# Optimization experiments

Hardware: AMD Instinct MI355X
Metric: run time of the kernel (lower is better)

The kernel has to match this reference:

```python
import jax, jax.numpy as jnp
import numpy as np

S, B, D, H = 1024, 16, 512, 8
DH = D // H  # 64


def setup_inputs() -> dict:
    key = jax.random.key(0)
    k1, k2, k3, k4, k5 = jax.random.split(key, 5)
    x = jax.random.normal(k1, (S, B, D), dtype=jnp.float32)
    # binary validity mask [B, S]: 1 = keep, 0 = masked out (matches torch usage)
    mask = (jax.random.uniform(k2, (B, S)) > 0.2).astype(jnp.float32)
    scale = 1.0 / np.sqrt(D)
    wq = jax.random.normal(k3, (H, DH, D), dtype=jnp.float32) * scale
    wk = jax.random.normal(k4, (H, DH, D), dtype=jnp.float32) * scale
    wv = jax.random.normal(k5, (H, DH, D), dtype=jnp.float32) * scale
    return {"x": x, "mask": mask, "wq": wq, "wk": wk, "wv": wv}


def reference(x, mask, wq, wk, wv):
    # x: [S, B, D]; mask: [B, S]; w*: [H, DH, D] (stacked bias-free Linear weights)
    dh = wq.shape[1]
    # per-hop projections for all hops at once (Linear: y = x @ W.T)
    q = jnp.einsum('sbd,hed->bhse', x, wq)  # [B,H,S,DH]
    k = jnp.einsum('sbd,hed->bhse', x, wk)
    v = jnp.einsum('sbd,hed->bhse', x, wv)
    scores = jnp.einsum('bhse,bhte->bhst', q, k)  # [B,H,S,S]
    inv_mask = (1.0 - mask)[:, None, None, :]      # broadcast over heads, query pos
    align = jnp.tanh(scores / jnp.sqrt(jnp.asarray(dh, x.dtype))) - 10000.0 * inv_mask
    align = jax.nn.softmax(align, axis=-1)
    out = jnp.einsum('bhst,bhte->bhse', align, v)  # [B,H,S,DH]
    s, b = x.shape[0], x.shape[1]
    # concat hops along feature dim, back to seq-first: [S, B, H*DH]
    return jnp.transpose(out, (2, 0, 1, 3)).reshape(s, b, -1)
```

## Files before the change

### kernel.cpp

```cpp
#include <hip/hip_runtime.h>
#include <stdint.h>
#include <stddef.h>

#define SS 1024
#define BB 16
#define DD 512
#define HH 8
#define DHH 64

typedef __attribute__((ext_vector_type(8))) short bf16x8;
typedef __attribute__((ext_vector_type(4))) float f32x4;
typedef __attribute__((ext_vector_type(16))) float f32x16;
typedef __attribute__((ext_vector_type(4))) float float4v;
typedef __attribute__((ext_vector_type(4))) unsigned short us4;

__device__ __forceinline__ unsigned short f2bf(float f) {
  union { float f; unsigned int u; } v; v.f = f;
  unsigned int x = v.u;
  return (unsigned short)((x + 0x7FFFu + ((x >> 16) & 1u)) >> 16);
}

#define GLDS16(dst, src)                                                                  \
  __builtin_amdgcn_global_load_lds(                                                      \
      (const __attribute__((address_space(1))) unsigned int*)(const void*)(src),         \
      (__attribute__((address_space(3))) unsigned int*)(void*)(dst), 16, 0, 0)

__global__ void cvt_kernel(const float* __restrict__ x,
                           const float* __restrict__ wq,
                           const float* __restrict__ wk,
                           const float* __restrict__ wv,
                           const float* __restrict__ mask,
                           unsigned short* __restrict__ xb,
                           unsigned short* __restrict__ wb,
                           float* __restrict__ maskq) {
  const int i = blockIdx.x * 256 + threadIdx.x;
  const int n_x4 = (SS * BB * DD) / 4;
  const int n_w4 = 3 * 65536;
  if (i < n_x4) {
    float4v v = ((const float4v*)x)[i];
    us4 o;
    o[0] = f2bf(v[0]); o[1] = f2bf(v[1]); o[2] = f2bf(v[2]); o[3] = f2bf(v[3]);
    ((us4*)xb)[i] = o;
  } else if (i < n_x4 + n_w4) {
    const int j = i - n_x4;
    const int sel = j >> 16;
    const int off4 = j & 65535;
    const float* wsrc = (sel == 0) ? wq : ((sel == 1) ? wk : wv);
    const float scale = (sel == 0) ? 0.36067376022224085f : 1.0f;
    float4v v = ((const float4v*)wsrc)[off4];
    us4 o;
    o[0] = f2bf(v[0] * scale); o[1] = f2bf(v[1] * scale);
    o[2] = f2bf(v[2] * scale); o[3] = f2bf(v[3] * scale);
    ((us4*)wb)[(sel << 16) + off4] = o;
  } else {
    const int j = i - n_x4 - n_w4;
    float4v mv = ((const float4v*)mask)[j];
    float4v o;
#pragma unroll
    for (int c = 0; c < 4; ++c) o[c] = (mv[c] > 0.5f) ? 0.f : -16384.f;
    ((float4v*)maskq)[j] = o;
  }
}

__global__ __launch_bounds__(256) void proj_kernel(
    const unsigned short* __restrict__ xb,
    const unsigned short* __restrict__ wb,
    unsigned short* __restrict__ qb,
    unsigned short* __restrict__ kb,
    unsigned short* __restrict__ vt) {
  const int bm = blockIdx.x * 128;
  const int bn = blockIdx.y * 128;
  const int b = blockIdx.z / 3;
  const int wsel = blockIdx.z % 3;

  __shared__ unsigned short At[128 * 32];
  __shared__ unsigned short Bt[128 * 32];
  __shared__ unsigned short OT[4][64 * 72];

  const int tid = threadIdx.x;
  const int w = tid >> 6;
  const int lane = tid & 63;

  const unsigned short* wptr = wb + wsel * (512 * DD);

  f32x4 acc[4][4];
#pragma unroll
  for (int mi = 0; mi < 4; ++mi)
#pragma unroll
    for (int ni = 0; ni < 4; ++ni) acc[mi][ni] = (f32x4){0.f, 0.f, 0.f, 0.f};

  const int m0 = (w & 1) * 64;
  const int n0 = (w >> 1) * 64;

  for (int kt = 0; kt < 16; ++kt) {
#pragma unroll
    for (int i = 0; i < 2; ++i) {
      const int idx8 = i * 256 + tid;
      const int r = idx8 >> 2;
      const int c8 = idx8 & 3;
      GLDS16(&At[(i * 256 + w * 64) * 8],
             xb + (size_t)(bm + r) * (BB * DD) + b * DD + kt * 32 + c8 * 8);
      GLDS16(&Bt[(i * 256 + w * 64) * 8],
             wptr + (size_t)(bn + r) * DD + kt * 32 + c8 * 8);
    }
    __syncthreads();
    bf16x8 af[4], bfr[4];
#pragma unroll
    for (int mi = 0; mi < 4; ++mi)
      af[mi] = *(const bf16x8*)&At[(m0 + mi * 16 + (lane & 15)) * 32 + (lane >> 4) * 8];
#pragma unroll
    for (int ni = 0; ni < 4; ++ni)
      bfr[ni] = *(const bf16x8*)&Bt[(n0 + ni * 16 + (lane & 15)) * 32 + (lane >> 4) * 8];
#pragma unroll
    for (int mi = 0; mi < 4; ++mi)
#pragma unroll
      for (int ni = 0; ni < 4; ++ni)
        acc[mi][ni] =
            __builtin_amdgcn_mfma_f32_16x16x32_bf16(af[mi], bfr[ni], acc[mi][ni], 0, 0, 0);
    __syncthreads();
  }

  const int h = (bn + n0) >> 6;
  unsigned short* OTw = &OT[w][0];
  if (wsel != 2) {
#pragma unroll
    for (int mi = 0; mi < 4; ++mi)
#pragma unroll
      for (int ni = 0; ni < 4; ++ni)
#pragma unroll
        for (int j = 0; j < 4; ++j)
          OTw[(mi * 16 + (lane >> 4) * 4 + j) * 72 + ni * 16 + (lane & 15)] =
              f2bf(acc[mi][ni][j]);
  } else {
#pragma unroll
    for (int mi = 0; mi < 4; ++mi)
#pragma unroll
      for (int ni = 0; ni < 4; ++ni) {
        us4 pk;
#pragma unroll
        for (int j = 0; j < 4; ++j) pk[j] = f2bf(acc[mi][ni][j]);
        *(us4*)&OTw[(ni * 16 + (lane & 15)) * 72 + mi * 16 + (lane >> 4) * 4] = pk;
      }
  }
  unsigned short* gout = (wsel == 0) ? qb : ((wsel == 1) ? kb : vt);
#pragma unroll
  for (int pass = 0; pass < 8; ++pass) {
    const int row = pass * 8 + (lane >> 3);
    bf16x8 vrow = *(const bf16x8*)&OTw[row * 72 + (lane & 7) * 8];
    size_t dst;
    if (wsel != 2)
      dst = ((size_t)(b * HH + h) * SS + (size_t)(bm + m0 + row)) * DHH + (lane & 7) * 8;
    else
      dst = ((size_t)(b * HH + h) * DHH + (size_t)row) * SS + (bm + m0) + (lane & 7) * 8;
    *(bf16x8*)&gout[dst] = vrow;
  }
}

__global__ __launch_bounds__(256, 4) void attn_kernel(
    const unsigned short* __restrict__ qb,
    const unsigned short* __restrict__ kb,
    const unsigned short* __restrict__ vt,
    const float* __restrict__ maskq,
    float* __restrict__ out) {
  const int id = blockIdx.x;
  const int xcd = id & 7;
  const int slot = id >> 3;
  const int bh = xcd * 16 + (slot >> 3);
  const int qt = slot & 7;
  const int b = bh >> 3;
  const int h = bh & 7;
  const int tid = threadIdx.x;
  const int w = tid >> 6;
  const int lane = tid & 63;
  const int l31 = lane & 31;
  const int hi32 = lane >> 5;

  __shared__ unsigned short Ks[2][64 * 64];
  __shared__ unsigned short Vs[2][64 * 64];
  __shared__ float rs_s[4][32];

  const size_t base_qk = (size_t)bh * SS * DHH;
  const int q0 = qt * 128 + w * 32;

  bf16x8 aq[4];
  {
    const unsigned short* qp = qb + base_qk + (size_t)(q0 + l31) * DHH + hi32 * 8;
    aq[0] = *(const bf16x8*)(qp);
    aq[1] = *(const bf16x8*)(qp + 16);
    aq[2] = *(const bf16x8*)(qp + 32);
    aq[3] = *(const bf16x8*)(qp + 48);
  }

  const int sr0 = w * 16 + (lane >> 3);
  const int sxb = (((lane & 7) ^ (lane >> 3)) << 4);
  const unsigned short* ksrc0 = kb + base_qk + (size_t)sr0 * DHH + (sxb >> 1);
  const unsigned short* ksrc1 = ksrc0 + 8 * DHH;
  const unsigned short* vsrc0 =
      vt + (size_t)bh * DHH * SS + (size_t)sr0 * SS + (sxb >> 1);
  const unsigned short* vsrc1 = vsrc0 + 8 * SS;

#define STAGE(bb, kt2)                                                       \
  do {                                                                       \
    GLDS16(&Ks[bb][(w * 16) * 64], ksrc0 + (size_t)(kt2) * (64 * DHH));      \
    GLDS16(&Ks[bb][(w * 16 + 8) * 64], ksrc1 + (size_t)(kt2) * (64 * DHH));  \
    GLDS16(&Vs[bb][(w * 16) * 64], vsrc0 + (size_t)(kt2) * 64);              \
    GLDS16(&Vs[bb][(w * 16 + 8) * 64], vsrc1 + (size_t)(kt2) * 64);          \
  } while (0)

  STAGE(0, 0);

  f32x16 accO[2];
#pragma unroll
  for (int n = 0; n < 2; ++n)
#pragma unroll
    for (int i = 0; i < 16; ++i) accO[n][i] = 0.f;
  float rs = 0.f;
  const float* mrow = maskq + b * SS;

  __syncthreads();

  int buf = 0;
  for (int kt = 0; kt < 16; ++kt) {
    if (kt < 15) STAGE(buf ^ 1, kt + 1);
    const char* Kb = (const char*)&Ks[buf][0];
    const char* Vb = (const char*)&Vs[buf][0];

#pragma unroll
    for (int T = 0; T < 2; ++T) {
      const int krow = T * 32 + l31;
      const int ksw = (krow & 7) << 4;
      f32x16 sc = {};
#pragma unroll
      for (int ks = 0; ks < 4; ++ks) {
        bf16x8 kf = *(const bf16x8*)(Kb + krow * 128 + ((ks * 32 + hi32 * 16) ^ ksw));
        sc = __builtin_amdgcn_mfma_f32_32x32x16_bf16(kf, aq[ks], sc, 0, 0, 0);
      }
      unsigned int pu[16];
#pragma unroll
      for (int g = 0; g < 4; ++g) {
        float4v mv = *(const float4v*)&mrow[kt * 64 + T * 32 + g * 8 + hi32 * 4];
#pragma unroll
        for (int i = 0; i < 4; ++i) {
          float u = __builtin_amdgcn_exp2f(sc[g * 4 + i]);
          float r = __builtin_amdgcn_rcpf(1.f + u);
          float p = __builtin_amdgcn_exp2f(__builtin_fmaf(r, -2.88539008178f, mv[i]));
          rs += p;
          union { float f; unsigned int u; } cv;
          cv.f = p;
          pu[g * 4 + i] = cv.u;
        }
      }
      unsigned int wv[8];
#pragma unroll
      for (int m = 0; m < 8; ++m)
        wv[m] = __builtin_amdgcn_perm(pu[2 * m + 1], pu[2 * m], 0x07060302u);
      unsigned int t0 = hi32 ? wv[0] : wv[2];
      unsigned int t1 = hi32 ? wv[1] : wv[3];
      unsigned int t2 = hi32 ? wv[4] : wv[6];
      unsigned int t3 = hi32 ? wv[5] : wv[7];
      unsigned int s0 = (unsigned int)__shfl_xor((int)t0, 32, 64);
      unsigned int s1 = (unsigned int)__shfl_xor((int)t1, 32, 64);
      unsigned int s2 = (unsigned int)__shfl_xor((int)t2, 32, 64);
      unsigned int s3 = (unsigned int)__shfl_xor((int)t3, 32, 64);
      union { unsigned int u[4]; bf16x8 v; } f0, f1;
      f0.u[0] = hi32 ? s0 : wv[0];
      f0.u[1] = hi32 ? s1 : wv[1];
      f0.u[2] = hi32 ? wv[2] : s0;
      f0.u[3] = hi32 ? wv[3] : s1;
      f1.u[0] = hi32 ? s2 : wv[4];
      f1.u[1] = hi32 ? s3 : wv[5];
      f1.u[2] = hi32 ? wv[6] : s2;
      f1.u[3] = hi32 ? wv[7] : s3;
#pragma unroll
      for (int n = 0; n < 2; ++n) {
        const int vrow = n * 32 + l31;
        const int vsw = (vrow & 7) << 4;
        bf16x8 bv0 = *(const bf16x8*)(Vb + vrow * 128 + (((T * 2 + 0) * 32 + hi32 * 16) ^ vsw));
        bf16x8 bv1 = *(const bf16x8*)(Vb + vrow * 128 + (((T * 2 + 1) * 32 + hi32 * 16) ^ vsw));
        accO[n] = __builtin_amdgcn_mfma_f32_32x32x16_bf16(f0.v, bv0, accO[n], 0, 0, 0);
        accO[n] = __builtin_amdgcn_mfma_f32_32x32x16_bf16(f1.v, bv1, accO[n], 0, 0, 0);
      }
    }
    __syncthreads();
    buf ^= 1;
  }
#undef STAGE

  rs += __shfl_xor(rs, 32, 64);
  if (hi32 == 0) rs_s[w][l31] = __builtin_amdgcn_rcpf(rs);
  float4v ri[4];
#pragma unroll
  for (int g = 0; g < 4; ++g) ri[g] = *(const float4v*)&rs_s[w][g * 8 + hi32 * 4];

#pragma unroll
  for (int n = 0; n < 2; ++n)
#pragma unroll
    for (int g = 0; g < 4; ++g)
#pragma unroll
      for (int i = 0; i < 4; ++i) {
        const int qrow = q0 + g * 8 + hi32 * 4 + i;
        out[((size_t)qrow * BB + b) * DD + h * DHH + n * 32 + l31] =
            accO[n][g * 4 + i] * ri[g][i];
      }
}

extern "C" void kernel_launch(void* const* d_in, const int* in_sizes, int n_in,
                              void* d_out, int out_size, void* d_ws, size_t ws_size,
                              hipStream_t stream) {
  const float* x = (const float*)d_in[0];
  const float* mask = (const float*)d_in[1];
  const float* wq = (const float*)d_in[2];
  const float* wk = (const float*)d_in[3];
  const float* wv = (const float*)d_in[4];
  float* out = (float*)d_out;

  char* ws = (char*)d_ws;
  unsigned short* xb = (unsigned short*)(ws);
  unsigned short* wb = (unsigned short*)(ws + (16ull << 20));
  float* maskq = (float*)(ws + (17ull << 20) + (512ull << 10));
  unsigned short* qb = (unsigned short*)(ws + (18ull << 20));
  unsigned short* kb = (unsigned short*)(ws + (34ull << 20));
  unsigned short* vt = (unsigned short*)(ws + (50ull << 20));

  cvt_kernel<<<dim3(8976), 256, 0, stream>>>(x, wq, wk, wv, mask, xb, wb, maskq);
  proj_kernel<<<dim3(8, 4, 48), 256, 0, stream>>>(xb, wb, qb, kb, vt);
  attn_kernel<<<dim3(1024), 256, 0, stream>>>(qb, kb, vt, maskq, out);
}
```

Before: 120.2 us.

## Permute K rows to drop shuffles, batch reciprocals, add MFMA priority hints

K rows are loaded in a permuted order (swapping bits 2 and 3 of the row index), so each lane's score accumulator already matches the operand layout the PV MFMA expects. That removes the cross-half-wave shuffles and selects before the second matmul, and the mask loads are reindexed to match. The four per-element reciprocals in the tanh step are replaced by one reciprocal plus multiplies (Montgomery batching). s_setprio is raised around the MFMA blocks to favour matrix issue across waves. Batching the reciprocals can lose some precision or overflow if the product of the (1+exp) terms becomes very large.

```diff
diff --git a/kernel.cpp b/kernel.cpp
--- a/kernel.cpp
+++ b/kernel.cpp
@@ -174,6 +174,7 @@
   const int lane = tid & 63;
   const int l31 = lane & 31;
   const int hi32 = lane >> 5;
+  const int sl = (l31 & 0x13) | ((l31 & 4) << 1) | ((l31 & 8) >> 1);
 
   __shared__ unsigned short Ks[2][64 * 64];
   __shared__ unsigned short Vs[2][64 * 64];
@@ -227,50 +228,46 @@
 
 #pragma unroll
     for (int T = 0; T < 2; ++T) {
-      const int krow = T * 32 + l31;
+      const int krow = T * 32 + sl;
       const int ksw = (krow & 7) << 4;
       f32x16 sc = {};
+      __builtin_amdgcn_s_setprio(1);
 #pragma unroll
       for (int ks = 0; ks < 4; ++ks) {
         bf16x8 kf = *(const bf16x8*)(Kb + krow * 128 + ((ks * 32 + hi32 * 16) ^ ksw));
         sc = __builtin_amdgcn_mfma_f32_32x32x16_bf16(kf, aq[ks], sc, 0, 0, 0);
       }
+      __builtin_amdgcn_s_setprio(0);
       unsigned int pu[16];
 #pragma unroll
       for (int g = 0; g < 4; ++g) {
-        float4v mv = *(const float4v*)&mrow[kt * 64 + T * 32 + g * 8 + hi32 * 4];
+        float4v mv = *(const float4v*)&mrow[kt * 64 + T * 32 + (g >> 1) * 16 +
+                                            hi32 * 8 + (g & 1) * 4];
+        float a0 = 1.f + __builtin_amdgcn_exp2f(sc[g * 4 + 0]);
+        float a1 = 1.f + __builtin_amdgcn_exp2f(sc[g * 4 + 1]);
+        float a2 = 1.f + __builtin_amdgcn_exp2f(sc[g * 4 + 2]);
+        float a3 = 1.f + __builtin_amdgcn_exp2f(sc[g * 4 + 3]);
+        float p01 = a0 * a1, p23 = a2 * a3;
+        float rq = __builtin_amdgcn_rcpf(p01 * p23);
+        float r01 = p23 * rq, r23 = p01 * rq;
+        float r[4];
+        r[0] = a1 * r01; r[1] = a0 * r01; r[2] = a3 * r23; r[3] = a2 * r23;
 #pragma unroll
         for (int i = 0; i < 4; ++i) {
-          float u = __builtin_amdgcn_exp2f(sc[g * 4 + i]);
-          float r = __builtin_amdgcn_rcpf(1.f + u);
-          float p = __builtin_amdgcn_exp2f(__builtin_fmaf(r, -2.88539008178f, mv[i]));
+          float p = __builtin_amdgcn_exp2f(__builtin_fmaf(r[i], -2.88539008178f, mv[i]));
           rs += p;
           union { float f; unsigned int u; } cv;
           cv.f = p;
           pu[g * 4 + i] = cv.u;
         }
       }
-      unsigned int wv[8];
-#pragma unroll
-      for (int m = 0; m < 8; ++m)
-        wv[m] = __builtin_amdgcn_perm(pu[2 * m + 1], pu[2 * m], 0x07060302u);
-      unsigned int t0 = hi32 ? wv[0] : wv[2];
-      unsigned int t1 = hi32 ? wv[1] : wv[3];
-      unsigned int t2 = hi32 ? wv[4] : wv[6];
-      unsigned int t3 = hi32 ? wv[5] : wv[7];
-      unsigned int s0 = (unsigned int)__shfl_xor((int)t0, 32, 64);
-      unsigned int s1 = (unsigned int)__shfl_xor((int)t1, 32, 64);
-      unsigned int s2 = (unsigned int)__shfl_xor((int)t2, 32, 64);
-      unsigned int s3 = (unsigned int)__shfl_xor((int)t3, 32, 64);
       union { unsigned int u[4]; bf16x8 v; } f0, f1;
-      f0.u[0] = hi32 ? s0 : wv[0];
-      f0.u[1] = hi32 ? s1 : wv[1];
-      f0.u[2] = hi32 ? wv[2] : s0;
-      f0.u[3] = hi32 ? wv[3] : s1;
-      f1.u[0] = hi32 ? s2 : wv[4];
-      f1.u[1] = hi32 ? s3 : wv[5];
-      f1.u[2] = hi32 ? wv[6] : s2;
-      f1.u[3] = hi32 ? wv[7] : s3;
+#pragma unroll
+      for (int m = 0; m < 4; ++m) {
+        f0.u[m] = __builtin_amdgcn_perm(pu[2 * m + 1], pu[2 * m], 0x07060302u);
+        f1.u[m] = __builtin_amdgcn_perm(pu[8 + 2 * m + 1], pu[8 + 2 * m], 0x07060302u);
+      }
+      __builtin_amdgcn_s_setprio(1);
 #pragma unroll
       for (int n = 0; n < 2; ++n) {
         const int vrow = n * 32 + l31;
@@ -280,6 +277,7 @@
         accO[n] = __builtin_amdgcn_mfma_f32_32x32x16_bf16(f0.v, bv0, accO[n], 0, 0, 0);
         accO[n] = __builtin_amdgcn_mfma_f32_32x32x16_bf16(f1.v, bv1, accO[n], 0, 0, 0);
       }
+      __builtin_amdgcn_s_setprio(0);
     }
     __syncthreads();
     buf ^= 1;
```

Result: faster. 116.4 us (-3.2%).
